# Kernel optimization log

Measured on AMD Instinct MI355X. Metric: run time of the kernel, lower is better.

The kernel has to match this reference:

```python
import jax, jax.numpy as jnp
import numpy as np

# Dims (match init_kwargs)
B, N, D_MODEL = 64, 64, 512
D_STATE = 512
D_ATT = D_MODEL
H, W, C, K = 128, 128, 16, 5
T = 32  # num_steps
HALF = K // 2


def _lin(key, out_d, in_d):
    kw, kb = jax.random.split(key)
    w = jax.random.normal(kw, (out_d, in_d), jnp.float32) * 0.02
    b = jax.random.normal(kb, (out_d,), jnp.float32) * 0.02
    return w, b


def setup_inputs() -> dict:
    key = jax.random.key(0)
    ks = jax.random.split(key, 12)
    token_reps = jax.random.normal(ks[0], (B, N, D_MODEL), jnp.float32)
    global_rep = jax.random.normal(ks[1], (B, D_MODEL), jnp.float32)
    attention_mask = jnp.ones((B, N), jnp.int32)
    w_init, b_init = _lin(ks[2], D_STATE, D_MODEL)
    wq, bq = _lin(ks[3], D_ATT, D_STATE)
    wk, bk = _lin(ks[4], D_ATT, D_MODEL)
    wv, bv = _lin(ks[5], D_ATT, D_MODEL)
    gru_in = D_ATT + D_MODEL
    w_ih, b_ih = _lin(ks[6], 3 * D_STATE, gru_in)
    w_hh, b_hh = _lin(ks[7], 3 * D_STATE, D_STATE)
    w_write, b_write = _lin(ks[8], C * K * K, D_STATE + D_ATT)
    w_loc, b_loc = _lin(ks[9], 3, D_STATE + D_ATT + D_MODEL)
    return dict(token_reps=token_reps, global_rep=global_rep, attention_mask=attention_mask,
                w_init=w_init, b_init=b_init, wq=wq, bq=bq, wk=wk, bk=bk, wv=wv, bv=bv,
                w_ih=w_ih, b_ih=b_ih, w_hh=w_hh, b_hh=b_hh,
                w_write=w_write, b_write=b_write, w_loc=w_loc, b_loc=b_loc)


def _forward(token_reps, global_rep, attention_mask,
             w_init, b_init, wq, bq, wk, bk, wv, bv,
             w_ih, b_ih, w_hh, b_hh, w_write, b_write, w_loc, b_loc):
    Bv = token_reps.shape[0]
    # Precompute keys/values (constant over steps)
    k_tok = token_reps @ wk.T + bk  # [B,N,d_att]
    v_tok = token_reps @ wv.T + bv  # [B,N,d_att]
    invalid = attention_mask == 0

    s0 = jnp.tanh(global_rep @ w_init.T + b_init)  # [B,d_state]
    # Padded canvas (NHWC): full KxK patches always fit; crop at the end
    # reproduces the torch clipped-window write exactly.
    canvas0 = jnp.zeros((Bv, H + 2 * HALF, W + 2 * HALF, C), jnp.float32)
    b_idx = jnp.arange(Bv)
    koff = jnp.arange(K)

    def step(carry, _):
        s, canvas_p = carry
        q = s @ wq.T + bq  # [B,d_att]
        scores = jnp.einsum('bd,bnd->bn', q, k_tok)
        scores = jnp.where(invalid, -1e9, scores)
        alpha = jax.nn.softmax(scores, axis=-1)
        r = jnp.einsum('bn,bnd->bd', alpha, v_tok)  # [B,d_att]
        # GRUCell (torch gate order r,z,n)
        x = jnp.concatenate([r, global_rep], axis=-1)
        gi = x @ w_ih.T + b_ih
        gh = s @ w_hh.T + b_hh
        ir, iz, inn = jnp.split(gi, 3, axis=-1)
        hr, hz, hn = jnp.split(gh, 3, axis=-1)
        rg = jax.nn.sigmoid(ir + hr)
        zg = jax.nn.sigmoid(iz + hz)
        ng = jnp.tanh(inn + rg * hn)
        s_new = (1.0 - zg) * ng + zg * s
        # Write patch
        patch = (jnp.concatenate([s_new, r], axis=-1) @ w_write.T + b_write)
        patch = patch.reshape(Bv, C, K, K).transpose(0, 2, 3, 1)  # [B,K,K,C]
        loc = jnp.concatenate([s_new, r, global_rep], axis=-1) @ w_loc.T + b_loc
        cx = jnp.tanh(loc[:, 0])
        cy = jnp.tanh(loc[:, 1])
        j = jnp.clip(jnp.round(0.5 * (cx + 1.0) * (W - 1)), 0, W - 1).astype(jnp.int32)
        i = jnp.clip(jnp.round(0.5 * (cy + 1.0) * (H - 1)), 0, H - 1).astype(jnp.int32)
        # padded coords: top-left of window in padded canvas is (i, j)
        rows = i[:, None] + koff  # [B,K]
        cols = j[:, None] + koff  # [B,K]
        canvas_p = canvas_p.at[b_idx[:, None, None], rows[:, :, None], cols[:, None, :]].add(patch)
        return (s_new, canvas_p), None

    (_, canvas_p), _ = jax.lax.scan(step, (s0, canvas0), None, length=T)
    canvas = canvas_p[:, HALF:HALF + H, HALF:HALF + W, :].transpose(0, 3, 1, 2)  # [B,C,H,W]
    return canvas


def reference(token_reps, global_rep, attention_mask,
              w_init, b_init, wq, bq, wk, bk, wv, bv,
              w_ih, b_ih, w_hh, b_hh, w_write, b_write, w_loc, b_loc):
    return _forward(token_reps, global_rep, attention_mask,
                    w_init, b_init, wq, bq, wk, bk, wv, bv,
                    w_ih, b_ih, w_hh, b_hh, w_write, b_write, w_loc, b_loc)
```

## Files before the change

### kernel.cpp

```cpp
#include <hip/hip_runtime.h>

#define BB 64
#define DD 512
#define TT 32

__device__ __forceinline__ float dot4(const float4 a, const float4 b) {
  return a.x * b.x + a.y * b.y + a.z * b.z + a.w * b.w;
}

__device__ __forceinline__ void cst(float* p, float v) {
  __hip_atomic_store(p, v, __ATOMIC_RELAXED, __HIP_MEMORY_SCOPE_AGENT);
}

__global__ __launch_bounds__(256) void setup_k(
    const float* __restrict__ wq, const float* __restrict__ bq,
    const float* __restrict__ wk, const float* __restrict__ bk,
    const float* __restrict__ tok, const float* __restrict__ grep,
    const float* __restrict__ w_ih, const float* __restrict__ b_ih,
    const float* __restrict__ w_init, const float* __restrict__ b_init,
    const float* __restrict__ w_loc, const float* __restrict__ b_loc,
    float* __restrict__ kqb, float* __restrict__ cbn, float* __restrict__ gig,
    float* __restrict__ sbuf, float* __restrict__ locg,
    float* __restrict__ aqkp, unsigned* __restrict__ bar) {
  __shared__ __align__(16) float As[16][132];
  __shared__ __align__(16) float Bs[16][68];
  const int blk = blockIdx.x, tid = threadIdx.x;

  if (blk < 128) {
    const int tx = tid & 15, ty = tid >> 4;
    const int m0 = (blk & 3) * 128, n0 = ((blk >> 2) & 7) * 64, zz = blk >> 5;
    float acc[8][4];
#pragma unroll
    for (int i = 0; i < 8; ++i)
#pragma unroll
      for (int j = 0; j < 4; ++j) acc[i][j] = 0.f;
    for (int k0 = zz * 128; k0 < zz * 128 + 128; k0 += 16) {
      {
        const int kk = tid >> 4, mseg = tid & 15;
        const float* ap = wq + (long)(k0 + kk) * 512 + m0 + mseg * 8;
        *(float4*)&As[kk][mseg * 8] = *(const float4*)ap;
        *(float4*)&As[kk][mseg * 8 + 4] = *(const float4*)(ap + 4);
      }
      {
        const int kk = tid >> 4, nq = tid & 15;
        *(float4*)&Bs[kk][nq * 4] = *(const float4*)(wk + (long)(k0 + kk) * 512 + n0 + nq * 4);
      }
      __syncthreads();
#pragma unroll
      for (int kk = 0; kk < 16; ++kk) {
        const float4 a0 = *(const float4*)&As[kk][ty * 8];
        const float4 a1 = *(const float4*)&As[kk][ty * 8 + 4];
        const float4 b0 = *(const float4*)&Bs[kk][tx * 4];
        const float am[8] = {a0.x, a0.y, a0.z, a0.w, a1.x, a1.y, a1.z, a1.w};
#pragma unroll
        for (int i = 0; i < 8; ++i) {
          acc[i][0] += am[i] * b0.x; acc[i][1] += am[i] * b0.y;
          acc[i][2] += am[i] * b0.z; acc[i][3] += am[i] * b0.w;
        }
      }
      __syncthreads();
    }
    float* Ce = aqkp + (long)zz * 262144;
#pragma unroll
    for (int i = 0; i < 8; ++i) {
      const int m = m0 + ty * 8 + i;
      *(float4*)&Ce[(long)m * 512 + n0 + tx * 4] =
          make_float4(acc[i][0], acc[i][1], acc[i][2], acc[i][3]);
    }
  } else if (blk < 130) {
    const int d = (blk - 128) * 256 + tid;
    float s = 0.f;
    for (int e = 0; e < DD; ++e) s += wq[e * DD + d] * bk[e];
    kqb[d] = s;
  } else if (blk < 146) {
    float* wkb = &As[0][0];
    float* red = &Bs[0][0];
    for (int k = tid; k < 512; k += 256) {
      float s = 0.f;
      for (int e = 0; e < DD; ++e) s += bq[e] * wk[e * DD + k];
      wkb[k] = s;
    }
    red[tid] = bq[tid] * bk[tid] + bq[tid + 256] * bk[tid + 256];
    __syncthreads();
    for (int s2 = 128; s2; s2 >>= 1) {
      if (tid < s2) red[tid] += red[tid + s2];
      __syncthreads();
    }
    const float bqbk = red[0];
    const int m = (blk - 130) * 256 + tid;
    const float* tr = tok + (long)m * 512;
    float acc = bqbk;
    for (int e = 0; e < 512; e += 8) {
      acc += dot4(*(const float4*)(tr + e), *(const float4*)(wkb + e));
      acc += dot4(*(const float4*)(tr + e + 4), *(const float4*)(wkb + e + 4));
    }
    cbn[m] = acc;
  } else if (blk < 170) {
    const int o = (blk - 146) * 64 + (tid & 63);
    const int b0 = (tid >> 6) * 16;
    float acc[16];
#pragma unroll
    for (int i = 0; i < 16; ++i) acc[i] = 0.f;
    const float* wr = w_ih + (long)o * 1024 + 512;
    for (int e = 0; e < 512; e += 4) {
      const float4 w4 = *(const float4*)(wr + e);
#pragma unroll
      for (int i = 0; i < 16; ++i)
        acc[i] += dot4(*(const float4*)(grep + (long)(b0 + i) * 512 + e), w4);
    }
    const float bi = b_ih[o];
#pragma unroll
    for (int i = 0; i < 16; ++i)
      gig[(long)(b0 + i) * 1536 + o] = acc[i] + bi;
  } else if (blk < 178) {
    const int d = (blk - 170) * 64 + (tid & 63);
    const int b0 = (tid >> 6) * 16;
    float acc[16];
#pragma unroll
    for (int i = 0; i < 16; ++i) acc[i] = 0.f;
    const float* wr = w_init + (long)d * 512;
    for (int e = 0; e < 512; e += 4) {
      const float4 w4 = *(const float4*)(wr + e);
#pragma unroll
      for (int i = 0; i < 16; ++i)
        acc[i] += dot4(*(const float4*)(grep + (long)(b0 + i) * 512 + e), w4);
    }
    const float bi = b_init[d];
#pragma unroll
    for (int i = 0; i < 16; ++i)
      sbuf[(long)(b0 + i) * 512 + d] = tanhf(acc[i] + bi);
  } else if (blk == 178) {
    if (tid < 128) {
      const int b = tid >> 1, j = tid & 1;
      const float* wr = w_loc + (long)j * 1536 + 1024;
      const float* gr = grep + (long)b * 512;
      float acc = b_loc[j];
      for (int e = 0; e < 512; e += 4)
        acc += dot4(*(const float4*)(gr + e), *(const float4*)(wr + e));
      locg[b * 2 + j] = acc;
    }
  } else {
    if (tid < 16)
      __hip_atomic_store(bar + tid * 64, 0u, __ATOMIC_RELAXED, __HIP_MEMORY_SCOPE_AGENT);
    __hip_atomic_store(bar + 1024 + tid * 32, 0u, __ATOMIC_RELAXED, __HIP_MEMORY_SCOPE_AGENT);
  }
}

__global__ __launch_bounds__(256) void dual2_k(
    const float* __restrict__ A, const float* __restrict__ aqkp,
    const float* __restrict__ bias0, float* __restrict__ C0,
    const float* __restrict__ B1, const float* __restrict__ bias1, float* __restrict__ C1) {
  __shared__ __align__(16) float As[16][132];
  __shared__ __align__(16) float Bs[16][68];
  const int tid = threadIdx.x;
  const int tx = tid & 15, ty = tid >> 4;
  const int m0 = blockIdx.x * 128, n0 = blockIdx.y * 64;
  const int z = blockIdx.z;
  const float* bias = z ? bias1 : bias0;
  float* C = z ? C1 : C0;
  float acc[8][4];
#pragma unroll
  for (int i = 0; i < 8; ++i)
#pragma unroll
    for (int j = 0; j < 4; ++j) acc[i][j] = 0.f;

  for (int k0 = 0; k0 < 512; k0 += 16) {
    {
      const int row = tid >> 1, half = tid & 1;
      const float* ap = A + (long)(m0 + row) * 512 + k0 + half * 8;
      const float4 a0 = *(const float4*)ap;
      const float4 a1 = *(const float4*)(ap + 4);
      const int kb = half * 8;
      As[kb + 0][row] = a0.x; As[kb + 1][row] = a0.y; As[kb + 2][row] = a0.z; As[kb + 3][row] = a0.w;
      As[kb + 4][row] = a1.x; As[kb + 5][row] = a1.y; As[kb + 6][row] = a1.z; As[kb + 7][row] = a1.w;
    }
    {
      const int n = tid >> 2, q = tid & 3;
      float4 b0;
      if (z == 0) {
        const float* pb = aqkp + (long)(n0 + n) * 512 + k0 + q * 4;
        const float4 p0 = *(const float4*)pb;
        const float4 p1 = *(const float4*)(pb + 262144);
        const float4 p2 = *(const float4*)(pb + 524288);
        const float4 p3 = *(const float4*)(pb + 786432);
        b0 = make_float4(p0.x + p1.x + p2.x + p3.x, p0.y + p1.y + p2.y + p3.y,
                         p0.z + p1.z + p2.z + p3.z, p0.w + p1.w + p2.w + p3.w);
      } else {
        b0 = *(const float4*)(B1 + (long)(n0 + n) * 512 + k0 + q * 4);
      }
      Bs[q * 4 + 0][n] = b0.x; Bs[q * 4 + 1][n] = b0.y; Bs[q * 4 + 2][n] = b0.z; Bs[q * 4 + 3][n] = b0.w;
    }
    __syncthreads();
#pragma unroll
    for (int kk = 0; kk < 16; ++kk) {
      const float4 a0 = *(const float4*)&As[kk][ty * 8];
      const float4 a1 = *(const float4*)&As[kk][ty * 8 + 4];
      const float4 b0 = *(const float4*)&Bs[kk][tx * 4];
      const float am[8] = {a0.x, a0.y, a0.z, a0.w, a1.x, a1.y, a1.z, a1.w};
#pragma unroll
      for (int i = 0; i < 8; ++i) {
        acc[i][0] += am[i] * b0.x; acc[i][1] += am[i] * b0.y;
        acc[i][2] += am[i] * b0.z; acc[i][3] += am[i] * b0.w;
      }
    }
    __syncthreads();
  }
  const float4 bvv = *(const float4*)(bias + n0 + tx * 4);
#pragma unroll
  for (int i = 0; i < 8; ++i) {
    const int m = m0 + ty * 8 + i;
    float4 v = make_float4(acc[i][0] + bvv.x, acc[i][1] + bvv.y, acc[i][2] + bvv.z, acc[i][3] + bvv.w);
    *(float4*)&C[(long)m * 512 + n0 + tx * 4] = v;
  }
}

__device__ __forceinline__ void grid_barrier(unsigned* __restrict__ bar, unsigned gen) {
  __syncthreads();
  const int blk = blockIdx.x, tid = threadIdx.x;
  unsigned* gctr = bar;
  unsigned* rel = bar + 1024;
  if (blk == 0) {
    if (tid == 0)
      __hip_atomic_fetch_add(gctr, 1u, __ATOMIC_RELAXED, __HIP_MEMORY_SCOPE_AGENT);
    if (tid < 16) {
      while (__hip_atomic_load(gctr + tid * 64, __ATOMIC_RELAXED, __HIP_MEMORY_SCOPE_AGENT) < gen * 16u)
        __builtin_amdgcn_s_sleep(1);
    }
    __syncthreads();
    __hip_atomic_store(rel + tid * 32, gen, __ATOMIC_RELAXED, __HIP_MEMORY_SCOPE_AGENT);
  } else {
    if (tid == 0) {
      __hip_atomic_fetch_add(gctr + (blk >> 4) * 64, 1u, __ATOMIC_RELAXED, __HIP_MEMORY_SCOPE_AGENT);
      while (__hip_atomic_load(rel + blk * 32, __ATOMIC_RELAXED, __HIP_MEMORY_SCOPE_AGENT) < gen)
        __builtin_amdgcn_s_sleep(1);
    }
  }
  __syncthreads();
}

__global__ __launch_bounds__(256, 1) void loop_k(
    const float* __restrict__ ktil, const float* __restrict__ cbn,
    const float* __restrict__ vt, const float* __restrict__ locg,
    float* __restrict__ sbuf, float* __restrict__ rbuf,
    const float* __restrict__ w_write, const float* __restrict__ b_write,
    const float* __restrict__ w_loc, const int* __restrict__ amask,
    float* __restrict__ patchbuf, float* __restrict__ locbuf,
    const float* __restrict__ gig, const float* __restrict__ w_ih,
    const float* __restrict__ w_hh, const float* __restrict__ b_hh,
    unsigned* __restrict__ bar) {
  __shared__ __align__(16) float sm_s[9216];
  __shared__ __align__(16) float sm_rr[9216];
  __shared__ __align__(16) float sm_g[832];
  __shared__ __align__(16) float sm_sc[64];
  __shared__ __align__(16) float sm_val[192];
  __shared__ __align__(16) float wpl[12288];
  float* sm_act = sm_rr;

  const int blk = blockIdx.x, tid = threadIdx.x, lane = tid & 63;
  const bool is_attn = (blk < 64);
  const bool is_patch = (blk >= 64) && (blk < 224);
  unsigned nsync = 0;

  int p_rg = 0, p_bg = 0;
  if (is_patch) {
    const int g = blk - 64;
    p_bg = g & 3; p_rg = g >> 2;
    for (int idx = tid; idx < 3072; idx += 256) {
      const int rho = idx >> 8, f4 = idx & 255;
      const int col = f4 << 2;
      const int cc2 = col >> 5, jj = (col >> 2) & 7;
      const int dcol = (cc2 << 5) | ((jj ^ (cc2 & 7)) << 2);
      const float* src = (rho < 10) ? (w_write + (long)(p_rg * 10 + rho) * 1024 + col)
                                    : (w_loc + (long)(rho - 10) * 1536 + col);
      *(float4*)(wpl + rho * 1024 + dcol) = *(const float4*)src;
    }
  }

  float4 wg[3][8];
  const int g_dg = blk & 63, g_bg = blk >> 6;
  {
    const int c = tid & 15, sl = tid >> 4;
#pragma unroll
    for (int i = 0; i < 3; ++i) {
      const int rho = sl * 3 + i;
      const float* wsrc;
      if (rho < 24) {
        const int g2 = rho >> 3, di = rho & 7;
        wsrc = w_ih + (long)(g2 * 512 + g_dg * 8 + di) * 1024 + c * 32;
      } else {
        const int rh = rho - 24, g2 = rh >> 3, di = rh & 7;
        wsrc = w_hh + (long)(g2 * 512 + g_dg * 8 + di) * 512 + c * 32;
      }
#pragma unroll
      for (int j = 0; j < 8; ++j) wg[i][j] = *(const float4*)(wsrc + 4 * j);
    }
  }
  __syncthreads();

  for (int t = 0; t <= TT; ++t) {
    const float* s_cur = sbuf + (long)t * (BB * DD);
    float* r_cur = rbuf + (long)t * (BB * DD);
    const float* r_prev = r_cur - BB * DD;

    if (t < TT) {
      const int sb2 = tid >> 4, ch = tid & 15;
      const int b = g_bg * 16 + sb2;
      const float* sp = s_cur + (long)b * DD + ch * 32;
      float* dsd = sm_s + sb2 * 576 + ch * 36;
#pragma unroll
      for (int jj = 0; jj < 8; ++jj)
        *(float4*)(dsd + 4 * jj) = *(const float4*)(sp + 4 * jj);
    }

    if (is_attn) {
      if (t < TT) {
        const int b = blk, wrp = tid >> 6;
        const float* sb = s_cur + (long)b * DD;
        const float4 sva = *(const float4*)(sb + lane * 8);
        const float4 svb = *(const float4*)(sb + lane * 8 + 4);
        for (int h8 = 0; h8 < 2; ++h8) {
          const float* kbase = ktil + ((long)(b * 64 + wrp * 16 + h8 * 8)) * DD + lane * 8;
          float4 ka[8], kb2[8];
#pragma unroll
          for (int i = 0; i < 8; ++i) {
            ka[i] = *(const float4*)(kbase + (long)i * DD);
            kb2[i] = *(const float4*)(kbase + (long)i * DD + 4);
          }
#pragma unroll
          for (int i = 0; i < 8; ++i) {
            float p = dot4(ka[i], sva) + dot4(kb2[i], svb);
#pragma unroll
            for (int off = 32; off; off >>= 1) p += __shfl_xor(p, off);
            if (lane == 0) {
              const int n = wrp * 16 + h8 * 8 + i;
              float sc = p + cbn[b * 64 + n];
              if (amask[b * 64 + n] == 0) sc = -1e9f;
              sm_sc[n] = sc;
            }
          }
        }
        __syncthreads();
        if (tid < 64) {
          const float v = sm_sc[tid];
          float m = v;
#pragma unroll
          for (int off = 32; off; off >>= 1) m = fmaxf(m, __shfl_xor(m, off));
          const float e = expf(v - m);
          float l2 = e;
#pragma unroll
          for (int off = 32; off; off >>= 1) l2 += __shfl_xor(l2, off);
          sm_sc[tid] = e / l2;
        }
        __syncthreads();
        float rx = 0.f, ry = 0.f;
        const float* vb = vt + (long)b * 64 * DD + (tid << 1);
        for (int n0 = 0; n0 < 64; n0 += 8) {
          float2 vv[8];
#pragma unroll
          for (int i = 0; i < 8; ++i)
            vv[i] = *(const float2*)(vb + (long)(n0 + i) * DD);
#pragma unroll
          for (int i = 0; i < 8; ++i) {
            const float a = sm_sc[n0 + i];
            rx = fmaf(a, vv[i].x, rx);
            ry = fmaf(a, vv[i].y, ry);
          }
        }
        cst(r_cur + (long)b * DD + (tid << 1), rx);
        cst(r_cur + (long)b * DD + (tid << 1) + 1, ry);
      }
    } else if (is_patch) {
      if (t >= 1) {
        const int c = tid & 31, sl = tid >> 5;
        const int tr = sl & 3, bgsub = sl >> 2;
        for (int h = 0; h < 2; ++h) {
          __syncthreads();
          {
            const int b_i8 = tid >> 5, l = tid & 31;
            const int b = p_bg * 16 + h * 8 + b_i8;
            const float* sp = s_cur + (long)b * DD + l * 16;
            const float* rp = r_prev + (long)b * DD + l * 16;
            float* dsd = sm_act + b_i8 * 1152 + (l >> 1) * 36 + (l & 1) * 16;
            float* drd = sm_act + b_i8 * 1152 + (16 + (l >> 1)) * 36 + (l & 1) * 16;
#pragma unroll
            for (int jj = 0; jj < 4; ++jj) {
              *(float4*)(dsd + 4 * jj) = *(const float4*)(sp + 4 * jj);
              *(float4*)(drd + 4 * jj) = *(const float4*)(rp + 4 * jj);
            }
          }
          __syncthreads();
          float4 wreg[3][8];
#pragma unroll
          for (int i = 0; i < 3; ++i) {
            const float* wrow = wpl + (tr * 3 + i) * 1024 + (c << 5);
#pragma unroll
            for (int j = 0; j < 8; ++j)
              wreg[i][j] = *(const float4*)(wrow + ((j ^ (c & 7)) << 2));
          }
          for (int bi = 0; bi < 4; ++bi) {
            const int bl = bgsub * 4 + bi;
            const int babs = p_bg * 16 + h * 8 + bl;
            const float* ap = sm_act + bl * 1152 + c * 36;
            float a0 = 0.f, a1 = 0.f, a2 = 0.f;
#pragma unroll
            for (int j = 0; j < 8; ++j) {
              const float4 av = *(const float4*)(ap + 4 * j);
              a0 += dot4(wreg[0][j], av);
              a1 += dot4(wreg[1][j], av);
              a2 += dot4(wreg[2][j], av);
            }
#pragma unroll
            for (int m = 1; m < 32; m <<= 1) {
              a0 += __shfl_xor(a0, m);
              a1 += __shfl_xor(a1, m);
              a2 += __shfl_xor(a2, m);
            }
            if (c == 0) {
              const int bslot = h * 8 + bl;
              const float av3[3] = {a0, a1, a2};
#pragma unroll
              for (int i = 0; i < 3; ++i) {
                const int rho = tr * 3 + i;
                float v = av3[i];
                if (rho >= 10) v += locg[babs * 2 + (rho - 10)];
                sm_val[rho * 16 + bslot] = v;
              }
            }
          }
        }
        __syncthreads();
        const int u = t - 1;
        if (tid < 160) {
          const int ri = tid >> 4, bl2 = tid & 15;
          const int row = p_rg * 10 + ri;
          const int b = p_bg * 16 + bl2;
          patchbuf[((long)u * 64 + b) * 400 + row] = sm_val[ri * 16 + bl2] + b_write[row];
        }
        if (p_rg == 0 && tid < 16) {
          const int b = p_bg * 16 + tid;
          const float lx = sm_val[160 + tid];
          const float ly = sm_val[176 + tid];
          const int jx = min(127, max(0, (int)rintf(0.5f * (tanhf(lx) + 1.f) * 127.f)));
          const int iy = min(127, max(0, (int)rintf(0.5f * (tanhf(ly) + 1.f) * 127.f)));
          locbuf[((long)u * 64 + b) * 2] = (float)jx;
          locbuf[((long)u * 64 + b) * 2 + 1] = (float)iy;
        }
      }
    }

    if (t == TT) break;

    grid_barrier(bar, ++nsync);

    {
      float* s_nxt = sbuf + (long)(t + 1) * (BB * DD);
      const int c = tid & 15, sl = tid >> 4;
      {
        const int sb2 = tid >> 4, ch = tid & 15;
        const int b = g_bg * 16 + sb2;
        const float* rp = r_cur + (long)b * DD + ch * 32;
        float* drd = sm_rr + sb2 * 576 + ch * 36;
#pragma unroll
        for (int jj = 0; jj < 8; ++jj)
          *(float4*)(drd + 4 * jj) = *(const float4*)(rp + 4 * jj);
      }
      __syncthreads();
      const float* base = (sl < 8) ? sm_rr : sm_s;
      for (int bl = 0; bl < 16; ++bl) {
        const float* ap = base + bl * 576 + c * 36;
        float a0 = 0.f, a1 = 0.f, a2 = 0.f;
#pragma unroll
        for (int j = 0; j < 8; ++j) {
          const float4 av = *(const float4*)(ap + 4 * j);
          a0 += dot4(wg[0][j], av);
          a1 += dot4(wg[1][j], av);
          a2 += dot4(wg[2][j], av);
        }
#pragma unroll
        for (int m = 1; m < 16; m <<= 1) {
          a0 += __shfl_xor(a0, m);
          a1 += __shfl_xor(a1, m);
          a2 += __shfl_xor(a2, m);
        }
        if (c == 0) {
          sm_g[bl * 52 + sl * 3 + 0] = a0;
          sm_g[bl * 52 + sl * 3 + 1] = a1;
          sm_g[bl * 52 + sl * 3 + 2] = a2;
        }
      }
      __syncthreads();
      if (tid < 128) {
        const int b_i = tid >> 3, di = tid & 7;
        const int b = g_bg * 16 + b_i, d = g_dg * 8 + di;
        const float ir = sm_g[b_i * 52 + di]        + gig[b * 1536 + d];
        const float iz = sm_g[b_i * 52 + 8 + di]    + gig[b * 1536 + 512 + d];
        const float in = sm_g[b_i * 52 + 16 + di]   + gig[b * 1536 + 1024 + d];
        const float hr = sm_g[b_i * 52 + 24 + di]   + b_hh[d];
        const float hz = sm_g[b_i * 52 + 32 + di]   + b_hh[512 + d];
        const float hn = sm_g[b_i * 52 + 40 + di]   + b_hh[1024 + d];
        const float rg2 = 1.f / (1.f + expf(-(ir + hr)));
        const float zg = 1.f / (1.f + expf(-(iz + hz)));
        const float ng = tanhf(in + rg2 * hn);
        const float sprev = s_cur[(long)b * DD + d];
        cst(s_nxt + (long)b * DD + d, (1.f - zg) * ng + zg * sprev);
      }
    }

    grid_barrier(bar, ++nsync);
  }
}

__global__ __launch_bounds__(256) void canvas_k(const float* __restrict__ pb,
                                                const float* __restrict__ lb,
                                                float* __restrict__ canvas) {
  __shared__ float ch[16384];
  const int blk = blockIdx.x, tid = threadIdx.x;
  const int b = blk >> 4, c = blk & 15;
  for (int i = tid; i < 4096; i += 256)
    ((float4*)ch)[i] = make_float4(0.f, 0.f, 0.f, 0.f);
  __syncthreads();
  for (int u = 0; u < TT; ++u) {
    const int jx = (int)lb[((long)u * 64 + b) * 2];
    const int iy = (int)lb[((long)u * 64 + b) * 2 + 1];
    if (tid < 25) {
      const float v = pb[((long)u * 64 + b) * 400 + c * 25 + tid];
      const int ki = tid / 5, kj = tid % 5;
      const int y = iy + ki - 2, x = jx + kj - 2;
      if (y >= 0 && y < 128 && x >= 0 && x < 128) ch[y * 128 + x] += v;
    }
    __syncthreads();
  }
  float* dst = canvas + ((long)b * 16 + c) * 16384;
  for (int i = tid; i < 4096; i += 256)
    ((float4*)dst)[i] = ((float4*)ch)[i];
}

extern "C" void kernel_launch(void* const* d_in, const int* in_sizes, int n_in,
                              void* d_out, int out_size, void* d_ws, size_t ws_size,
                              hipStream_t stream) {
  const float* tok     = (const float*)d_in[0];
  const float* grep    = (const float*)d_in[1];
  const int*   amask   = (const int*)d_in[2];
  const float* w_init  = (const float*)d_in[3];
  const float* b_init  = (const float*)d_in[4];
  const float* wq      = (const float*)d_in[5];
  const float* bq      = (const float*)d_in[6];
  const float* wk      = (const float*)d_in[7];
  const float* bk      = (const float*)d_in[8];
  const float* wv      = (const float*)d_in[9];
  const float* bv      = (const float*)d_in[10];
  const float* w_ih    = (const float*)d_in[11];
  const float* b_ih    = (const float*)d_in[12];
  const float* w_hh    = (const float*)d_in[13];
  const float* b_hh    = (const float*)d_in[14];
  const float* w_write = (const float*)d_in[15];
  const float* b_write = (const float*)d_in[16];
  const float* w_loc   = (const float*)d_in[17];
  const float* b_loc   = (const float*)d_in[18];
  float* canvas = (float*)d_out;

  float* ws = (float*)d_ws;
  float* ktil = ws;
  float* vtw  = ktil + 2097152;
  float* Aqk  = vtw + 2097152;
  float* gig  = Aqk + 262144;
  float* cbn  = gig + 98304;
  float* sbuf = cbn + 4096;
  float* rbuf = sbuf + 1081344;
  float* locg = rbuf + 1048576;
  float* kqb  = locg + 128;
  float* wkbq = kqb + 512;
  float* bqbk = wkbq + 512;
  unsigned* bar = (unsigned*)(bqbk + 64);
  float* patchbuf = (float*)(bar + 16384);
  float* locbuf = patchbuf + 819200;
  float* aqkp = rbuf;

  setup_k<<<180, 256, 0, stream>>>(wq, bq, wk, bk, tok, grep, w_ih, b_ih,
                                   w_init, b_init, w_loc, b_loc,
                                   kqb, cbn, gig, sbuf, locg, aqkp, bar);
  dual2_k<<<dim3(32, 8, 2), 256, 0, stream>>>(tok, aqkp, kqb, ktil, wv, bv, vtw);
  loop_k<<<256, 256, 0, stream>>>(ktil, cbn, vtw, locg, sbuf, rbuf, w_write, b_write,
                                  w_loc, amask, patchbuf, locbuf, gig, w_ih, w_hh, b_hh, bar);
  canvas_k<<<1024, 256, 0, stream>>>(patchbuf, locbuf, canvas);
}
```

Measured before the change: 1.074 ms.

## Compute GRU hidden-state gates before grid barrier and cache biases in shared memory

Moves the W_hh·s half of the GRU gate matvec out of the post-barrier phase and runs it before the grid barrier, since it depends only on the current state already in shared memory. Only the W_ih·r half now runs between the two barriers, which shortens the critical path between grid syncs. It also preloads the per-block gig and b_hh values into shared memory once and reads the previous state from shared memory instead of global. The risk is extra work on attention/patch blocks before the barrier, which could lengthen that phase.

```diff
diff --git a/kernel.cpp b/kernel.cpp
--- a/kernel.cpp
+++ b/kernel.cpp
@@ -253,6 +253,8 @@
   __shared__ __align__(16) float sm_g[832];
   __shared__ __align__(16) float sm_sc[64];
   __shared__ __align__(16) float sm_val[192];
+  __shared__ __align__(16) float sm_gig[384];
+  __shared__ __align__(16) float sm_bhh[24];
   __shared__ __align__(16) float wpl[12288];
   float* sm_act = sm_rr;
 
@@ -294,6 +296,19 @@
 #pragma unroll
       for (int j = 0; j < 8; ++j) wg[i][j] = *(const float4*)(wsrc + 4 * j);
     }
+  }
+  if (tid < 128) {
+    const int b_i = tid >> 3, di = tid & 7;
+    const int b = g_bg * 16 + b_i, d = g_dg * 8 + di;
+    sm_gig[tid * 3 + 0] = gig[(long)b * 1536 + d];
+    sm_gig[tid * 3 + 1] = gig[(long)b * 1536 + 512 + d];
+    sm_gig[tid * 3 + 2] = gig[(long)b * 1536 + 1024 + d];
+  }
+  if (tid < 8) {
+    const int d = g_dg * 8 + tid;
+    sm_bhh[tid * 3 + 0] = b_hh[d];
+    sm_bhh[tid * 3 + 1] = b_hh[512 + d];
+    sm_bhh[tid * 3 + 2] = b_hh[1024 + d];
   }
   __syncthreads();
 
@@ -448,6 +463,35 @@
       }
     }
 
+    if (t < TT) {
+      __syncthreads();
+      const int c = tid & 15, sl = tid >> 4;
+      if (sl >= 8) {
+        for (int bl = 0; bl < 16; ++bl) {
+          const float* ap = sm_s + bl * 576 + c * 36;
+          float a0 = 0.f, a1 = 0.f, a2 = 0.f;
+#pragma unroll
+          for (int j = 0; j < 8; ++j) {
+            const float4 av = *(const float4*)(ap + 4 * j);
+            a0 += dot4(wg[0][j], av);
+            a1 += dot4(wg[1][j], av);
+            a2 += dot4(wg[2][j], av);
+          }
+#pragma unroll
+          for (int m = 1; m < 16; m <<= 1) {
+            a0 += __shfl_xor(a0, m);
+            a1 += __shfl_xor(a1, m);
+            a2 += __shfl_xor(a2, m);
+          }
+          if (c == 0) {
+            sm_g[bl * 52 + sl * 3 + 0] = a0;
+            sm_g[bl * 52 + sl * 3 + 1] = a1;
+            sm_g[bl * 52 + sl * 3 + 2] = a2;
+          }
+        }
+      }
+    }
+
     if (t == TT) break;
 
     grid_barrier(bar, ++nsync);
@@ -465,43 +509,44 @@
           *(float4*)(drd + 4 * jj) = *(const float4*)(rp + 4 * jj);
       }
       __syncthreads();
-      const float* base = (sl < 8) ? sm_rr : sm_s;
-      for (int bl = 0; bl < 16; ++bl) {
-        const float* ap = base + bl * 576 + c * 36;
-        float a0 = 0.f, a1 = 0.f, a2 = 0.f;
-#pragma unroll
-        for (int j = 0; j < 8; ++j) {
-          const float4 av = *(const float4*)(ap + 4 * j);
-          a0 += dot4(wg[0][j], av);
-          a1 += dot4(wg[1][j], av);
-          a2 += dot4(wg[2][j], av);
-        }
-#pragma unroll
-        for (int m = 1; m < 16; m <<= 1) {
-          a0 += __shfl_xor(a0, m);
-          a1 += __shfl_xor(a1, m);
-          a2 += __shfl_xor(a2, m);
-        }
-        if (c == 0) {
-          sm_g[bl * 52 + sl * 3 + 0] = a0;
-          sm_g[bl * 52 + sl * 3 + 1] = a1;
-          sm_g[bl * 52 + sl * 3 + 2] = a2;
+      if (sl < 8) {
+        for (int bl = 0; bl < 16; ++bl) {
+          const float* ap = sm_rr + bl * 576 + c * 36;
+          float a0 = 0.f, a1 = 0.f, a2 = 0.f;
+#pragma unroll
+          for (int j = 0; j < 8; ++j) {
+            const float4 av = *(const float4*)(ap + 4 * j);
+            a0 += dot4(wg[0][j], av);
+            a1 += dot4(wg[1][j], av);
+            a2 += dot4(wg[2][j], av);
+          }
+#pragma unroll
+          for (int m = 1; m < 16; m <<= 1) {
+            a0 += __shfl_xor(a0, m);
+            a1 += __shfl_xor(a1, m);
+            a2 += __shfl_xor(a2, m);
+          }
+          if (c == 0) {
+            sm_g[bl * 52 + sl * 3 + 0] = a0;
+            sm_g[bl * 52 + sl * 3 + 1] = a1;
+            sm_g[bl * 52 + sl * 3 + 2] = a2;
+          }
         }
       }
       __syncthreads();
       if (tid < 128) {
         const int b_i = tid >> 3, di = tid & 7;
         const int b = g_bg * 16 + b_i, d = g_dg * 8 + di;
-        const float ir = sm_g[b_i * 52 + di]        + gig[b * 1536 + d];
-        const float iz = sm_g[b_i * 52 + 8 + di]    + gig[b * 1536 + 512 + d];
-        const float in = sm_g[b_i * 52 + 16 + di]   + gig[b * 1536 + 1024 + d];
-        const float hr = sm_g[b_i * 52 + 24 + di]   + b_hh[d];
-        const float hz = sm_g[b_i * 52 + 32 + di]   + b_hh[512 + d];
-        const float hn = sm_g[b_i * 52 + 40 + di]   + b_hh[1024 + d];
+        const float ir = sm_g[b_i * 52 + di]        + sm_gig[tid * 3 + 0];
+        const float iz = sm_g[b_i * 52 + 8 + di]    + sm_gig[tid * 3 + 1];
+        const float in = sm_g[b_i * 52 + 16 + di]   + sm_gig[tid * 3 + 2];
+        const float hr = sm_g[b_i * 52 + 24 + di]   + sm_bhh[di * 3 + 0];
+        const float hz = sm_g[b_i * 52 + 32 + di]   + sm_bhh[di * 3 + 1];
+        const float hn = sm_g[b_i * 52 + 40 + di]   + sm_bhh[di * 3 + 2];
         const float rg2 = 1.f / (1.f + expf(-(ir + hr)));
         const float zg = 1.f / (1.f + expf(-(iz + hz)));
         const float ng = tanhf(in + rg2 * hn);
-        const float sprev = s_cur[(long)b * DD + d];
+        const float sprev = sm_s[b_i * 576 + (d >> 5) * 36 + (d & 31)];
         cst(s_nxt + (long)b * DD + d, (1.f - zg) * ng + zg * sprev);
       }
     }
```

New measurement: 1.291 ms. 20.2% more time.
